# Optimization experiments

Hardware: AMD Instinct MI355X
Metric: run time of the kernel (lower is better)

## Reference

```python
import jax, jax.numpy as jnp
import numpy as np

B, S, HID = 2, 2048, 2048
N_HEADS, N_KV = 16, 8
HEAD_DIM = HID // N_HEADS  # 128
N_REP = N_HEADS // N_KV


def setup_inputs() -> dict:
    key = jax.random.key(0)
    ks = jax.random.split(key, 5)
    x = jax.random.normal(ks[0], (B, S, HID), dtype=jnp.float32)
    Wq = jax.random.normal(ks[1], (HID, N_HEADS * HEAD_DIM), dtype=jnp.float32) * 0.02
    Wk = jax.random.normal(ks[2], (HID, N_KV * HEAD_DIM), dtype=jnp.float32) * 0.02
    Wv = jax.random.normal(ks[3], (HID, N_KV * HEAD_DIM), dtype=jnp.float32) * 0.02
    Wo = jax.random.normal(ks[4], (N_HEADS * HEAD_DIM, HID), dtype=jnp.float32) * 0.02
    # standard RoPE frequencies: theta_i = 10000^(-2i/head_dim), angle = pos * theta_i
    inv_freq = 1.0 / (10000.0 ** (jnp.arange(0, HEAD_DIM, 2, dtype=jnp.float32) / HEAD_DIM))
    angles = jnp.arange(S, dtype=jnp.float32)[:, None] * inv_freq[None, :]  # [S, HEAD_DIM/2]
    return {
        "x": x, "Wq": Wq, "Wk": Wk, "Wv": Wv, "Wo": Wo,
        "freqs_cos": jnp.cos(angles), "freqs_sin": jnp.sin(angles),
        "start_pos": 0,
    }


def _rope(t, cos, sin):
    # t: [B, S, h, head_dim]; complex-view pairs are (even, odd) along last dim
    tr = t.reshape(*t.shape[:-1], -1, 2)
    re, im = tr[..., 0], tr[..., 1]
    cos = cos[None, :, None, :]
    sin = sin[None, :, None, :]
    out_re = re * cos - im * sin
    out_im = re * sin + im * cos
    return jnp.stack([out_re, out_im], axis=-1).reshape(t.shape)


def reference(x, Wq, Wk, Wv, Wo, freqs_cos, freqs_sin, start_pos):
    b, s, _ = x.shape
    xq = (x @ Wq).reshape(b, s, N_HEADS, HEAD_DIM)
    xk = (x @ Wk).reshape(b, s, N_KV, HEAD_DIM)
    xv = (x @ Wv).reshape(b, s, N_KV, HEAD_DIM)
    xq = _rope(xq, freqs_cos, freqs_sin)
    xk = _rope(xk, freqs_cos, freqs_sin)
    # repeat_kv: each kv head duplicated n_rep times consecutively
    xk = jnp.repeat(xk, N_REP, axis=2)  # [b, s, N_HEADS, hd]
    xv = jnp.repeat(xv, N_REP, axis=2)
    scale = 1.0 / jnp.sqrt(jnp.float32(HEAD_DIM))
    attn = jnp.einsum("bqhd,bkhd->bhqk", xq, xk) * scale
    attn = jax.nn.softmax(attn, axis=-1)
    out = jnp.einsum("bhqk,bkhd->bqhd", attn, xv).reshape(b, s, N_HEADS * HEAD_DIM)
    return out @ Wo
```

## Files before the change

### kernel.cpp

```cpp
#include <hip/hip_runtime.h>
#include <stdint.h>

#define DI __device__ __forceinline__

typedef unsigned short u16;
typedef unsigned int   u32;
typedef __attribute__((ext_vector_type(8))) short short8;
typedef __attribute__((ext_vector_type(4))) float f32x4;


DI u16 f2bf(float f) {
    u32 u = __float_as_uint(f);
    u32 r = u + 0x7fff + ((u >> 16) & 1);
    return (u16)(r >> 16);
}
DI u32 pk2bf(float a, float b) {
    return (u32)f2bf(a) | ((u32)f2bf(b) << 16);
}
DI float bf2f(u16 h) { return __uint_as_float(((u32)h) << 16); }

DI f32x4 mfma16(short8 a, short8 b, f32x4 c) {
    return __builtin_amdgcn_mfma_f32_16x16x32_bf16(a, b, c, 0, 0, 0);
}

DI void gload_lds16(const void* g, void* l) {
    __builtin_amdgcn_global_load_lds(
        (const __attribute__((address_space(1))) void*)g,
        (__attribute__((address_space(3))) void*)l, 16, 0, 0);
}

DI short8 rope8(short8 raw, const float* cp, const float* sp, float osc) {
    float4 c4 = *(const float4*)cp;
    float4 s4 = *(const float4*)sp;
    u32* rp = (u32*)&raw;
#pragma unroll
    for (int p = 0; p < 4; p++) {
        u32 v = rp[p];
        float re = __uint_as_float(v << 16);
        float im = __uint_as_float(v & 0xffff0000u);
        float cc = ((const float*)&c4)[p] * osc;
        float ss = ((const float*)&s4)[p] * osc;
        rp[p] = pk2bf(re * cc - im * ss, re * ss + im * cc);
    }
    return raw;
}

__global__ __launch_bounds__(256) void cvt_x(const float* __restrict__ x,
                                             u16* __restrict__ o, int n4) {
    int i = blockIdx.x * 256 + threadIdx.x;
    if (i >= n4) return;
    float4 v = *(const float4*)(x + (size_t)i * 4);
    uint2 p; p.x = pk2bf(v.x, v.y); p.y = pk2bf(v.z, v.w);
    *(uint2*)(o + (size_t)i * 4) = p;
}

__global__ __launch_bounds__(256) void transpose_cvt4(const float* __restrict__ W0,
                                                      const float* __restrict__ W1,
                                                      const float* __restrict__ W2,
                                                      const float* __restrict__ W3,
                                                      u16* __restrict__ D0,
                                                      u16* __restrict__ D1,
                                                      u16* __restrict__ D2,
                                                      u16* __restrict__ D3) {
    const float* W; u16* D; int N;
    switch (blockIdx.z) {
        case 0:  W = W0; D = D0; N = 2048; break;
        case 1:  W = W1; D = D1; N = 1024; break;
        case 2:  W = W2; D = D2; N = 1024; break;
        default: W = W3; D = D3; N = 2048; break;
    }
    if ((int)blockIdx.x >= (N >> 6)) return;
    const int K = 2048;
    __shared__ u16 tl[64][65];
    int tx = threadIdx.x & 15, ty = threadIdx.x >> 4;
    int tc = blockIdx.x * 64, tr = blockIdx.y * 64;
#pragma unroll
    for (int i = 0; i < 4; i++) {
        int r = tr + ty + i * 16;
        float4 v = *(const float4*)&W[(size_t)r * N + tc + tx * 4];
        tl[tx*4+0][ty+i*16] = f2bf(v.x);
        tl[tx*4+1][ty+i*16] = f2bf(v.y);
        tl[tx*4+2][ty+i*16] = f2bf(v.z);
        tl[tx*4+3][ty+i*16] = f2bf(v.w);
    }
    __syncthreads();
#pragma unroll
    for (int i = 0; i < 4; i++) {
        int n = tc + ty + i * 16;
        uint2 p;
        p.x = (u32)tl[ty+i*16][tx*4+0] | ((u32)tl[ty+i*16][tx*4+1] << 16);
        p.y = (u32)tl[ty+i*16][tx*4+2] | ((u32)tl[ty+i*16][tx*4+3] << 16);
        *(uint2*)&D[(size_t)n * K + tr + tx * 4] = p;
    }
}

__global__ __launch_bounds__(256) void rope_kernel(u16* __restrict__ buf,
                                                   const float* __restrict__ fc,
                                                   const float* __restrict__ fs,
                                                   int H, int tokshift, int total,
                                                   float oscale) {
    int idx = blockIdx.x * 256 + threadIdx.x;
    if (idx >= total) return;
    int tok = idx >> tokshift;
    int rem = idx & ((1 << tokshift) - 1);
    int h = rem >> 6, j = rem & 63;
    int s = tok & 2047;
    size_t a = ((size_t)tok * H + h) * 128 + 2 * j;
    u32 v = *(u32*)(buf + a);
    float re = bf2f((u16)(v & 0xffff));
    float im = bf2f((u16)(v >> 16));
    float c = fc[s * 64 + j], sn = fs[s * 64 + j];
    *(u32*)(buf + a) = pk2bf((re * c - im * sn) * oscale,
                             (re * sn + im * c) * oscale);
}

__global__ __launch_bounds__(512) void gemm_qkv8(const u16* __restrict__ A,
                                                 const u16* __restrict__ BT,
                                                 u16* __restrict__ Qo,
                                                 u16* __restrict__ Ko,
                                                 u16* __restrict__ Vo) {
    __shared__ __align__(16) u16 SM[65536];
    char* smb = (char*)SM;
    const int tid = threadIdx.x;
    const int w = tid >> 6, l = tid & 63;
    const int l15 = l & 15, lh = l >> 4;
    const int wr = w >> 2, wc = w & 3;

    const int bid = blockIdx.x;
    const int sw = (bid & 7) * 32 + (bid >> 3);
    const int bx = sw & 15, by = sw >> 4;

    const char* Ag = (const char*)A  + (size_t)(by * 256) * 4096;
    const char* Bg = (const char*)BT + (size_t)(bx * 256) * 4096;

    const int r0 = tid >> 3;
    const int c0 = ((tid & 7) << 4) ^ (((tid >> 5) & 1) << 5);
    const int wb = w << 10;

#define STG_A(tt, bb, hh) do {                                              \
        const char* s_ = Ag + (size_t)((hh) * 128 + r0) * 4096 + (tt) * 128 + c0; \
        char* d_ = smb + (bb) * 65536 + (hh) * 16384 + wb;                  \
        gload_lds16(s_, d_);                                                \
        gload_lds16(s_ + (size_t)64 * 4096, d_ + 8192);                     \
    } while (0)
#define STG_B(tt, bb, hh) do {                                              \
        const char* s_ = Bg + (size_t)((hh) * 128 + r0) * 4096 + (tt) * 128 + c0; \
        char* d_ = smb + (bb) * 65536 + 32768 + (hh) * 16384 + wb;          \
        gload_lds16(s_, d_);                                                \
        gload_lds16(s_ + (size_t)64 * 4096, d_ + 8192);                     \
    } while (0)

    const int aoff = l15 * 128 + ((lh * 16) ^ (((l15 >> 2) & 1) << 5));

    const f32x4 fz = {0.f, 0.f, 0.f, 0.f};
    f32x4 acc[8][4];
#pragma unroll
    for (int m = 0; m < 8; m++)
#pragma unroll
        for (int n = 0; n < 4; n++) acc[m][n] = fz;

    STG_A(0, 0, 0); STG_A(0, 0, 1); STG_B(0, 0, 0); STG_B(0, 0, 1);
    STG_A(1, 1, 0);
    asm volatile("s_waitcnt vmcnt(2)" ::: "memory");
    __builtin_amdgcn_s_barrier();

    for (int t = 0; t < 32; ++t) {
        const int cur = t & 1;
        const int t1 = t + 1 < 32 ? t + 1 : 31;
        const int t2 = t + 2 < 32 ? t + 2 : 31;
        const char* Ab = smb + cur * 65536 + wr * 16384 + aoff;
        const char* Bb = smb + cur * 65536 + 32768 + (wc >> 1) * 16384
                         + (wc & 1) * 8192 + aoff;
        short8 aF[4][2], bF[4][2];

        STG_A(t1, cur ^ 1, 1);
#pragma unroll
        for (int m = 0; m < 4; m++) {
            aF[m][0] = *(const short8*)(Ab + m * 2048);
            aF[m][1] = *(const short8*)(Ab + m * 2048 + 64);
        }
#pragma unroll
        for (int n = 0; n < 2; n++) {
            bF[n][0] = *(const short8*)(Bb + n * 2048);
            bF[n][1] = *(const short8*)(Bb + n * 2048 + 64);
        }
        __builtin_amdgcn_s_setprio(1);
#pragma unroll
        for (int m = 0; m < 4; m++)
#pragma unroll
            for (int n = 0; n < 2; n++) {
                acc[m][n] = mfma16(aF[m][0], bF[n][0], acc[m][n]);
                acc[m][n] = mfma16(aF[m][1], bF[n][1], acc[m][n]);
            }
        __builtin_amdgcn_s_setprio(0);
        __builtin_amdgcn_s_barrier();

        STG_B(t1, cur ^ 1, 0);
#pragma unroll
        for (int n = 2; n < 4; n++) {
            bF[n][0] = *(const short8*)(Bb + n * 2048);
            bF[n][1] = *(const short8*)(Bb + n * 2048 + 64);
        }
        __builtin_amdgcn_s_setprio(1);
#pragma unroll
        for (int m = 0; m < 4; m++)
#pragma unroll
            for (int n = 2; n < 4; n++) {
                acc[m][n] = mfma16(aF[m][0], bF[n][0], acc[m][n]);
                acc[m][n] = mfma16(aF[m][1], bF[n][1], acc[m][n]);
            }
        __builtin_amdgcn_s_setprio(0);
        __builtin_amdgcn_s_barrier();

        STG_B(t1, cur ^ 1, 1);
#pragma unroll
        for (int m = 0; m < 4; m++) {
            aF[m][0] = *(const short8*)(Ab + (m + 4) * 2048);
            aF[m][1] = *(const short8*)(Ab + (m + 4) * 2048 + 64);
        }
        __builtin_amdgcn_s_setprio(1);
#pragma unroll
        for (int m = 0; m < 4; m++)
#pragma unroll
            for (int n = 0; n < 2; n++) {
                acc[m + 4][n] = mfma16(aF[m][0], bF[n][0], acc[m + 4][n]);
                acc[m + 4][n] = mfma16(aF[m][1], bF[n][1], acc[m + 4][n]);
            }
        __builtin_amdgcn_s_setprio(0);
        __builtin_amdgcn_s_barrier();

        STG_A(t2, cur, 0);
        __builtin_amdgcn_s_setprio(1);
#pragma unroll
        for (int m = 0; m < 4; m++)
#pragma unroll
            for (int n = 2; n < 4; n++) {
                acc[m + 4][n] = mfma16(aF[m][0], bF[n][0], acc[m + 4][n]);
                acc[m + 4][n] = mfma16(aF[m][1], bF[n][1], acc[m + 4][n]);
            }
        __builtin_amdgcn_s_setprio(0);
        asm volatile("s_waitcnt vmcnt(2)" ::: "memory");
        __builtin_amdgcn_s_barrier();
    }
#undef STG_A
#undef STG_B

    const int rbase = by * 256 + wr * 128 + lh * 4;
    const int cbase = bx * 256 + wc * 64 + l15;
    if (bx < 8) {
#pragma unroll
        for (int m = 0; m < 8; m++)
#pragma unroll
            for (int j = 0; j < 4; j++) {
                size_t ro = (size_t)(rbase + m * 16 + j) * 2048 + cbase;
#pragma unroll
                for (int n = 0; n < 4; n++)
                    Qo[ro + n * 16] = f2bf(acc[m][n][j]);
            }
    } else if (bx < 12) {
        const int ck = cbase - 2048;
#pragma unroll
        for (int m = 0; m < 8; m++)
#pragma unroll
            for (int j = 0; j < 4; j++) {
                size_t ro = (size_t)(rbase + m * 16 + j) * 1024 + ck;
#pragma unroll
                for (int n = 0; n < 4; n++)
                    Ko[ro + n * 16] = f2bf(acc[m][n][j]);
            }
    } else {
#pragma unroll
        for (int m = 0; m < 8; m++)
#pragma unroll
            for (int n = 0; n < 4; n++) {
                int tok = rbase + m * 16;
                int c = cbase + n * 16 - 3072;
                int bb2 = tok >> 11, ss = tok & 2047;
                int h2 = c >> 7, d = c & 127;
                uint2 v;
                v.x = pk2bf(acc[m][n][0], acc[m][n][1]);
                v.y = pk2bf(acc[m][n][2], acc[m][n][3]);
                *(uint2*)(Vo + (size_t)((bb2 * 8 + h2) * 128 + d) * 2048 + ss) = v;
            }
    }
}

__global__ __launch_bounds__(512) void gemm_wo8(const u16* __restrict__ A,
                                                const u16* __restrict__ BT,
                                                float* __restrict__ Of) {
    __shared__ __align__(16) u16 SM[49152];
    char* smb = (char*)SM;
    const int tid = threadIdx.x;
    const int w = tid >> 6, l = tid & 63;
    const int l15 = l & 15, lh = l >> 4;
    const int wr = w >> 2, wc = w & 3;

    const int bid = blockIdx.x;
    const int sw = (bid & 7) * 32 + (bid >> 3);
    const int bx = sw & 7, by = sw >> 3;

    const char* Ag = (const char*)A  + (size_t)(by * 128) * 4096;
    const char* Bg = (const char*)BT + (size_t)(bx * 256) * 4096;

    const int r0 = tid >> 3;
    const int c0 = ((tid & 7) << 4) ^ (((tid >> 5) & 1) << 5);
    const int wb = w << 10;

#define STG_WA(tt, bb) do {                                                 \
        const char* s_ = Ag + (size_t)r0 * 4096 + (tt) * 128 + c0;          \
        char* d_ = smb + (bb) * 49152 + wb;                                 \
        gload_lds16(s_, d_);                                                \
        gload_lds16(s_ + (size_t)64 * 4096, d_ + 8192);                     \
    } while (0)
#define STG_WB(tt, bb) do {                                                 \
        const char* s_ = Bg + (size_t)r0 * 4096 + (tt) * 128 + c0;          \
        char* d_ = smb + (bb) * 49152 + 16384 + wb;                         \
        gload_lds16(s_, d_);                                                \
        gload_lds16(s_ + (size_t)64 * 4096, d_ + 8192);                     \
        gload_lds16(s_ + (size_t)128 * 4096, d_ + 16384);                   \
        gload_lds16(s_ + (size_t)192 * 4096, d_ + 24576);                   \
    } while (0)

    const int aoff = l15 * 128 + ((lh * 16) ^ (((l15 >> 2) & 1) << 5));

    const f32x4 fz = {0.f, 0.f, 0.f, 0.f};
    f32x4 acc[4][4];
#pragma unroll
    for (int m = 0; m < 4; m++)
#pragma unroll
        for (int n = 0; n < 4; n++) acc[m][n] = fz;

    STG_WA(0, 0); STG_WB(0, 0);
    STG_WA(1, 1);
    asm volatile("s_waitcnt vmcnt(2)" ::: "memory");
    __builtin_amdgcn_s_barrier();

    for (int t = 0; t < 32; ++t) {
        const int cur = t & 1;
        const int t1 = t + 1 < 32 ? t + 1 : 31;
        const int t2 = t + 2 < 32 ? t + 2 : 31;
        const char* Ab = smb + cur * 49152 + wr * 8192 + aoff;
        const char* Bb = smb + cur * 49152 + 16384 + wc * 8192 + aoff;
        short8 aF[4][2], bF[4][2];

        STG_WB(t1, cur ^ 1);
#pragma unroll
        for (int m = 0; m < 4; m++) {
            aF[m][0] = *(const short8*)(Ab + m * 2048);
            aF[m][1] = *(const short8*)(Ab + m * 2048 + 64);
        }
#pragma unroll
        for (int n = 0; n < 2; n++) {
            bF[n][0] = *(const short8*)(Bb + n * 2048);
            bF[n][1] = *(const short8*)(Bb + n * 2048 + 64);
        }
        __builtin_amdgcn_s_setprio(1);
#pragma unroll
        for (int m = 0; m < 4; m++)
#pragma unroll
            for (int n = 0; n < 2; n++) {
                acc[m][n] = mfma16(aF[m][0], bF[n][0], acc[m][n]);
                acc[m][n] = mfma16(aF[m][1], bF[n][1], acc[m][n]);
            }
        __builtin_amdgcn_s_setprio(0);
        __builtin_amdgcn_s_barrier();

        STG_WA(t2, cur);
#pragma unroll
        for (int n = 2; n < 4; n++) {
            bF[n][0] = *(const short8*)(Bb + n * 2048);
            bF[n][1] = *(const short8*)(Bb + n * 2048 + 64);
        }
        __builtin_amdgcn_s_setprio(1);
#pragma unroll
        for (int m = 0; m < 4; m++)
#pragma unroll
            for (int n = 2; n < 4; n++) {
                acc[m][n] = mfma16(aF[m][0], bF[n][0], acc[m][n]);
                acc[m][n] = mfma16(aF[m][1], bF[n][1], acc[m][n]);
            }
        __builtin_amdgcn_s_setprio(0);
        asm volatile("s_waitcnt vmcnt(2)" ::: "memory");
        __builtin_amdgcn_s_barrier();
    }
#undef STG_WA
#undef STG_WB

    const int rbase = by * 128 + wr * 64 + lh * 4;
    const int cbase = bx * 256 + wc * 64 + l15;
#pragma unroll
    for (int m = 0; m < 4; m++)
#pragma unroll
        for (int j = 0; j < 4; j++) {
            size_t ro = (size_t)(rbase + m * 16 + j) * 2048 + cbase;
#pragma unroll
            for (int n = 0; n < 4; n++)
                Of[ro + n * 16] = acc[m][n][j];
        }
}

__global__ __launch_bounds__(256, 2) void attn_kernel(const u16* __restrict__ Q,
                                                      const u16* __restrict__ Kg,
                                                      const u16* __restrict__ Vg,
                                                      const float* __restrict__ fc,
                                                      const float* __restrict__ fs,
                                                      u16* __restrict__ O) {
    __shared__ __align__(16) u16 Ks[2][8192];
    __shared__ __align__(16) u16 Vs[2][8192];
    __shared__ __align__(16) u16 Ps[4][2048];
    const int tid = threadIdx.x;
    const int w = tid >> 6, l = tid & 63;
    const int qt = blockIdx.x, bh = blockIdx.y;
    const int b = bh >> 4, h = bh & 15, h2 = h >> 1;
    const int l15 = l & 15, lh = l >> 4;

    char* KsB = (char*)&Ks[0][0];
    char* VsB = (char*)&Vs[0][0];
    char* PsB = (char*)&Ps[w][0];

    const char* Kbase = (const char*)Kg + (size_t)b * 2048 * 2048 + h2 * 256;
    const char* Vbase = (const char*)Vg + (size_t)(b * 8 + h2) * 128 * 4096;
    int krow[4], kcol[4], vrow[4], vcol[4];
#pragma unroll
    for (int c = 0; c < 4; c++) {
        int X = c * 4096 + tid * 16;
        krow[c] = X >> 8; kcol[c] = (X & 255) ^ ((krow[c] & 7) << 4);
        vrow[c] = X >> 7; vcol[c] = (X & 127) ^ ((vrow[c] & 7) << 4);
    }

#define STAGE(t, pb) do {                                               \
        const char* Kt = Kbase + (size_t)(t) * 131072;                  \
        const char* Vt = Vbase + (t) * 128;                             \
        char* kd = KsB + (pb) * 16384 + tid * 16;                       \
        char* vd = VsB + (pb) * 16384 + tid * 16;                       \
        _Pragma("unroll")                                               \
        for (int c = 0; c < 4; c++) {                                   \
            gload_lds16(Kt + krow[c] * 2048 + kcol[c], kd + c * 4096);  \
            gload_lds16(Vt + (size_t)vrow[c] * 4096 + vcol[c], vd + c * 4096); \
        }                                                               \
    } while (0)

    const float OSC = 0.12751742987f;
    short8 qf0[4], qf1[4];
    {
        const int s0r = qt * 128 + w * 32 + l15;
        const int s1r = s0r + 16;
        const u16* qp0 = Q + ((size_t)(b * 2048 + s0r)) * 2048 + h * 128 + lh * 8;
        const u16* qp1 = Q + ((size_t)(b * 2048 + s1r)) * 2048 + h * 128 + lh * 8;
#pragma unroll
        for (int ks = 0; ks < 4; ks++) {
            qf0[ks] = rope8(*(const short8*)(qp0 + ks * 32),
                            &fc[s0r * 64 + ks * 16 + lh * 4],
                            &fs[s0r * 64 + ks * 16 + lh * 4], OSC);
            qf1[ks] = rope8(*(const short8*)(qp1 + ks * 32),
                            &fc[s1r * 64 + ks * 16 + lh * 4],
                            &fs[s1r * 64 + ks * 16 + lh * 4], OSC);
        }
    }

    const f32x4 fz = {0.f, 0.f, 0.f, 0.f};
    f32x4 o0[8], o1[8];
#pragma unroll
    for (int n = 0; n < 8; n++) { o0[n] = fz; o1[n] = fz; }
    float mrow0[4] = {-1e30f, -1e30f, -1e30f, -1e30f};
    float mrow1[4] = {-1e30f, -1e30f, -1e30f, -1e30f};
    float lsum0[4] = {0.f, 0.f, 0.f, 0.f};
    float lsum1[4] = {0.f, 0.f, 0.f, 0.f};

    STAGE(0, 0);

    for (int t = 0; t < 32; t++) {
        __syncthreads();
        const int pb = t & 1;
        if (t < 31) STAGE(t + 1, pb ^ 1);
        const char* kc = KsB + pb * 16384;
        const char* vc = VsB + pb * 16384;
        const int swz = (l15 & 7) << 4;

        f32x4 s0[4], s1[4];
#pragma unroll
        for (int ct = 0; ct < 4; ct++) {
            s0[ct] = fz; s1[ct] = fz;
#pragma unroll
            for (int ks = 0; ks < 4; ks++) {
                short8 kf = *(const short8*)(kc + ((ct * 16 + l15) << 8)
                                                + ((ks * 64 + lh * 16) ^ swz));
                s0[ct] = mfma16(qf0[ks], kf, s0[ct]);
                s1[ct] = mfma16(qf1[ks], kf, s1[ct]);
            }
        }

        float pl0[4], pl1[4];
#pragma unroll
        for (int r = 0; r < 4; r++) {
            pl0[r] = fmaxf(fmaxf(s0[0][r], s0[1][r]), fmaxf(s0[2][r], s0[3][r]));
            pl1[r] = fmaxf(fmaxf(s1[0][r], s1[1][r]), fmaxf(s1[2][r], s1[3][r]));
        }
        bool grow = false;
#pragma unroll
        for (int r = 0; r < 4; r++)
            grow = grow || (pl0[r] > mrow0[r] + 8.f) || (pl1[r] > mrow1[r] + 8.f);
        if (__any(grow)) {
#pragma unroll
            for (int r = 0; r < 4; r++) {
                float mx = pl0[r];
                mx = fmaxf(mx, __shfl_xor(mx, 1));
                mx = fmaxf(mx, __shfl_xor(mx, 2));
                mx = fmaxf(mx, __shfl_xor(mx, 4));
                mx = fmaxf(mx, __shfl_xor(mx, 8));
                float mnew = fmaxf(mrow0[r], mx);
                float fsc = exp2f(mrow0[r] - mnew);
                mrow0[r] = mnew;
                lsum0[r] *= fsc;
#pragma unroll
                for (int n = 0; n < 8; n++) o0[n][r] *= fsc;
            }
#pragma unroll
            for (int r = 0; r < 4; r++) {
                float mx = pl1[r];
                mx = fmaxf(mx, __shfl_xor(mx, 1));
                mx = fmaxf(mx, __shfl_xor(mx, 2));
                mx = fmaxf(mx, __shfl_xor(mx, 4));
                mx = fmaxf(mx, __shfl_xor(mx, 8));
                float mnew = fmaxf(mrow1[r], mx);
                float fsc = exp2f(mrow1[r] - mnew);
                mrow1[r] = mnew;
                lsum1[r] *= fsc;
#pragma unroll
                for (int n = 0; n < 8; n++) o1[n][r] *= fsc;
            }
        }
        const int cb2 = l15 << 1;
#pragma unroll
        for (int r = 0; r < 4; r++) {
            float p0 = exp2f(s0[0][r] - mrow0[r]);
            float p1 = exp2f(s0[1][r] - mrow0[r]);
            float p2 = exp2f(s0[2][r] - mrow0[r]);
            float p3 = exp2f(s0[3][r] - mrow0[r]);
            lsum0[r] += (p0 + p1) + (p2 + p3);
            const int rw = lh * 4 + r;
            const int rb = rw << 7;
            const int sw2 = (rw & 7) << 4;
            *(u16*)(PsB + (rb + (( 0 + cb2) ^ sw2))) =
                (u16)((__float_as_uint(p0) + 0x8000u) >> 16);
            *(u16*)(PsB + (rb + ((32 + cb2) ^ sw2))) =
                (u16)((__float_as_uint(p1) + 0x8000u) >> 16);
            *(u16*)(PsB + (rb + ((64 + cb2) ^ sw2))) =
                (u16)((__float_as_uint(p2) + 0x8000u) >> 16);
            *(u16*)(PsB + (rb + ((96 + cb2) ^ sw2))) =
                (u16)((__float_as_uint(p3) + 0x8000u) >> 16);
        }
#pragma unroll
        for (int r = 0; r < 4; r++) {
            float p0 = exp2f(s1[0][r] - mrow1[r]);
            float p1 = exp2f(s1[1][r] - mrow1[r]);
            float p2 = exp2f(s1[2][r] - mrow1[r]);
            float p3 = exp2f(s1[3][r] - mrow1[r]);
            lsum1[r] += (p0 + p1) + (p2 + p3);
            const int rw = 16 + lh * 4 + r;
            const int rb = rw << 7;
            const int sw2 = (rw & 7) << 4;
            *(u16*)(PsB + (rb + (( 0 + cb2) ^ sw2))) =
                (u16)((__float_as_uint(p0) + 0x8000u) >> 16);
            *(u16*)(PsB + (rb + ((32 + cb2) ^ sw2))) =
                (u16)((__float_as_uint(p1) + 0x8000u) >> 16);
            *(u16*)(PsB + (rb + ((64 + cb2) ^ sw2))) =
                (u16)((__float_as_uint(p2) + 0x8000u) >> 16);
            *(u16*)(PsB + (rb + ((96 + cb2) ^ sw2))) =
                (u16)((__float_as_uint(p3) + 0x8000u) >> 16);
        }

#pragma unroll
        for (int ks2 = 0; ks2 < 2; ks2++) {
            short8 pf0 = *(const short8*)(PsB + ((l15 << 7)
                                + ((ks2 * 64 + lh * 16) ^ swz)));
            short8 pf1 = *(const short8*)(PsB + (((16 + l15) << 7)
                                + ((ks2 * 64 + lh * 16) ^ swz)));
#pragma unroll
            for (int n = 0; n < 8; n++) {
                short8 vf = *(const short8*)(vc + (((n * 16 + l15) << 7)
                                                  + ((ks2 * 64 + lh * 16) ^ swz)));
                o0[n] = mfma16(pf0, vf, o0[n]);
                o1[n] = mfma16(pf1, vf, o1[n]);
            }
        }
    }

    const int q0 = qt * 128 + w * 32;
    const size_t ob0 = ((size_t)(b * 2048 + q0 + lh * 4)) * 2048 + h * 128 + l15;
#pragma unroll
    for (int r = 0; r < 4; r++) {
        float ls = lsum0[r];
        ls += __shfl_xor(ls, 1);
        ls += __shfl_xor(ls, 2);
        ls += __shfl_xor(ls, 4);
        ls += __shfl_xor(ls, 8);
        float li = 1.0f / ls;
#pragma unroll
        for (int n = 0; n < 8; n++)
            O[ob0 + (size_t)r * 2048 + n * 16] = f2bf(o0[n][r] * li);
    }
    const size_t ob1 = ob0 + (size_t)16 * 2048;
#pragma unroll
    for (int r = 0; r < 4; r++) {
        float ls = lsum1[r];
        ls += __shfl_xor(ls, 1);
        ls += __shfl_xor(ls, 2);
        ls += __shfl_xor(ls, 4);
        ls += __shfl_xor(ls, 8);
        float li = 1.0f / ls;
#pragma unroll
        for (int n = 0; n < 8; n++)
            O[ob1 + (size_t)r * 2048 + n * 16] = f2bf(o1[n][r] * li);
    }
#undef STAGE
}

extern "C" void kernel_launch(void* const* d_in, const int* in_sizes, int n_in,
                              void* d_out, int out_size, void* d_ws, size_t ws_size,
                              hipStream_t stream) {
    const float* x  = (const float*)d_in[0];
    const float* Wq = (const float*)d_in[1];
    const float* Wk = (const float*)d_in[2];
    const float* Wv = (const float*)d_in[3];
    const float* Wo = (const float*)d_in[4];
    const float* fc = (const float*)d_in[5];
    const float* fs = (const float*)d_in[6];
    float* out = (float*)d_out;

    uint8_t* ws = (uint8_t*)d_ws;
    u16* xb   = (u16*)(ws + 0);
    u16* wqkv = (u16*)(ws + 16777216);
    u16* wqT  = (u16*)(ws + 16777216);
    u16* wkT  = (u16*)(ws + 25165824);
    u16* wvT  = (u16*)(ws + 29360128);
    u16* woT  = (u16*)(ws + 33554432);
    u16* qb   = (u16*)(ws + 41943040);
    u16* kb   = (u16*)(ws + 58720256);
    u16* vT   = (u16*)(ws + 67108864);
    u16* ao   = xb;

    cvt_x<<<dim3(8192), dim3(256), 0, stream>>>(x, xb, 2097152);
    transpose_cvt4<<<dim3(32, 32, 4), dim3(256), 0, stream>>>(Wq, Wk, Wv, Wo,
                                                              wqT, wkT, wvT, woT);

    gemm_qkv8<<<dim3(256), dim3(512), 0, stream>>>(xb, wqkv, qb, kb, vT);

    rope_kernel<<<dim3(8192), dim3(256), 0, stream>>>(kb, fc, fs, 8, 9, 2097152, 1.0f);

    attn_kernel<<<dim3(16, 32), dim3(256), 0, stream>>>(qb, kb, vT, fc, fs, ao);

    gemm_wo8<<<dim3(256), dim3(512), 0, stream>>>(ao, woT, out);
}
```

Baseline: 233.3 us.

## Shrink QKV GEMM tile to 128x256 and launch 512 blocks

The fused QKV projection GEMM tile drops from 256x256 to 128x256 rows per block, doubling the grid to 512 workgroups. Each block now stages one A half-tile and the full B tile per k-step, with two compute phases instead of four, and uses less LDS. The goal is to fill all 256 CUs more evenly and cut the wave-quantization tail. The cost is lower arithmetic intensity per block, so B-operand global and LDS traffic rises for each FLOP.

```diff
diff --git a/kernel.cpp b/kernel.cpp
--- a/kernel.cpp
+++ b/kernel.cpp
@@ -114,12 +114,12 @@
                              (re * sn + im * c) * oscale);
 }
 
-__global__ __launch_bounds__(512) void gemm_qkv8(const u16* __restrict__ A,
+__global__ __launch_bounds__(512) void gemm_qkv2(const u16* __restrict__ A,
                                                  const u16* __restrict__ BT,
                                                  u16* __restrict__ Qo,
                                                  u16* __restrict__ Ko,
                                                  u16* __restrict__ Vo) {
-    __shared__ __align__(16) u16 SM[65536];
+    __shared__ __align__(16) u16 SM[49152];
     char* smb = (char*)SM;
     const int tid = threadIdx.x;
     const int w = tid >> 6, l = tid & 63;
@@ -127,40 +127,42 @@
     const int wr = w >> 2, wc = w & 3;
 
     const int bid = blockIdx.x;
-    const int sw = (bid & 7) * 32 + (bid >> 3);
+    const int sw = (bid & 7) * 64 + (bid >> 3);
     const int bx = sw & 15, by = sw >> 4;
 
-    const char* Ag = (const char*)A  + (size_t)(by * 256) * 4096;
+    const char* Ag = (const char*)A  + (size_t)(by * 128) * 4096;
     const char* Bg = (const char*)BT + (size_t)(bx * 256) * 4096;
 
     const int r0 = tid >> 3;
     const int c0 = ((tid & 7) << 4) ^ (((tid >> 5) & 1) << 5);
     const int wb = w << 10;
 
-#define STG_A(tt, bb, hh) do {                                              \
-        const char* s_ = Ag + (size_t)((hh) * 128 + r0) * 4096 + (tt) * 128 + c0; \
-        char* d_ = smb + (bb) * 65536 + (hh) * 16384 + wb;                  \
+#define STG_WA(tt, bb) do {                                                 \
+        const char* s_ = Ag + (size_t)r0 * 4096 + (tt) * 128 + c0;          \
+        char* d_ = smb + (bb) * 49152 + wb;                                 \
         gload_lds16(s_, d_);                                                \
         gload_lds16(s_ + (size_t)64 * 4096, d_ + 8192);                     \
     } while (0)
-#define STG_B(tt, bb, hh) do {                                              \
-        const char* s_ = Bg + (size_t)((hh) * 128 + r0) * 4096 + (tt) * 128 + c0; \
-        char* d_ = smb + (bb) * 65536 + 32768 + (hh) * 16384 + wb;          \
+#define STG_WB(tt, bb) do {                                                 \
+        const char* s_ = Bg + (size_t)r0 * 4096 + (tt) * 128 + c0;          \
+        char* d_ = smb + (bb) * 49152 + 16384 + wb;                         \
         gload_lds16(s_, d_);                                                \
         gload_lds16(s_ + (size_t)64 * 4096, d_ + 8192);                     \
+        gload_lds16(s_ + (size_t)128 * 4096, d_ + 16384);                   \
+        gload_lds16(s_ + (size_t)192 * 4096, d_ + 24576);                   \
     } while (0)
 
     const int aoff = l15 * 128 + ((lh * 16) ^ (((l15 >> 2) & 1) << 5));
 
     const f32x4 fz = {0.f, 0.f, 0.f, 0.f};
-    f32x4 acc[8][4];
-#pragma unroll
-    for (int m = 0; m < 8; m++)
+    f32x4 acc[4][4];
+#pragma unroll
+    for (int m = 0; m < 4; m++)
 #pragma unroll
         for (int n = 0; n < 4; n++) acc[m][n] = fz;
 
-    STG_A(0, 0, 0); STG_A(0, 0, 1); STG_B(0, 0, 0); STG_B(0, 0, 1);
-    STG_A(1, 1, 0);
+    STG_WA(0, 0); STG_WB(0, 0);
+    STG_WA(1, 1);
     asm volatile("s_waitcnt vmcnt(2)" ::: "memory");
     __builtin_amdgcn_s_barrier();
 
@@ -168,12 +170,11 @@
         const int cur = t & 1;
         const int t1 = t + 1 < 32 ? t + 1 : 31;
         const int t2 = t + 2 < 32 ? t + 2 : 31;
-        const char* Ab = smb + cur * 65536 + wr * 16384 + aoff;
-        const char* Bb = smb + cur * 65536 + 32768 + (wc >> 1) * 16384
-                         + (wc & 1) * 8192 + aoff;
+        const char* Ab = smb + cur * 49152 + wr * 8192 + aoff;
+        const char* Bb = smb + cur * 49152 + 16384 + wc * 8192 + aoff;
         short8 aF[4][2], bF[4][2];
 
-        STG_A(t1, cur ^ 1, 1);
+        STG_WB(t1, cur ^ 1);
 #pragma unroll
         for (int m = 0; m < 4; m++) {
             aF[m][0] = *(const short8*)(Ab + m * 2048);
@@ -195,7 +196,7 @@
         __builtin_amdgcn_s_setprio(0);
         __builtin_amdgcn_s_barrier();
 
-        STG_B(t1, cur ^ 1, 0);
+        STG_WA(t2, cur);
 #pragma unroll
         for (int n = 2; n < 4; n++) {
             bF[n][0] = *(const short8*)(Bb + n * 2048);
@@ -210,46 +211,17 @@
                 acc[m][n] = mfma16(aF[m][1], bF[n][1], acc[m][n]);
             }
         __builtin_amdgcn_s_setprio(0);
-        __builtin_amdgcn_s_barrier();
-
-        STG_B(t1, cur ^ 1, 1);
-#pragma unroll
-        for (int m = 0; m < 4; m++) {
-            aF[m][0] = *(const short8*)(Ab + (m + 4) * 2048);
-            aF[m][1] = *(const short8*)(Ab + (m + 4) * 2048 + 64);
-        }
-        __builtin_amdgcn_s_setprio(1);
-#pragma unroll
-        for (int m = 0; m < 4; m++)
-#pragma unroll
-            for (int n = 0; n < 2; n++) {
-                acc[m + 4][n] = mfma16(aF[m][0], bF[n][0], acc[m + 4][n]);
-                acc[m + 4][n] = mfma16(aF[m][1], bF[n][1], acc[m + 4][n]);
-            }
-        __builtin_amdgcn_s_setprio(0);
-        __builtin_amdgcn_s_barrier();
-
-        STG_A(t2, cur, 0);
-        __builtin_amdgcn_s_setprio(1);
-#pragma unroll
-        for (int m = 0; m < 4; m++)
-#pragma unroll
-            for (int n = 2; n < 4; n++) {
-                acc[m + 4][n] = mfma16(aF[m][0], bF[n][0], acc[m + 4][n]);
-                acc[m + 4][n] = mfma16(aF[m][1], bF[n][1], acc[m + 4][n]);
-            }
-        __builtin_amdgcn_s_setprio(0);
         asm volatile("s_waitcnt vmcnt(2)" ::: "memory");
         __builtin_amdgcn_s_barrier();
     }
-#undef STG_A
-#undef STG_B
-
-    const int rbase = by * 256 + wr * 128 + lh * 4;
+#undef STG_WA
+#undef STG_WB
+
+    const int rbase = by * 128 + wr * 64 + lh * 4;
     const int cbase = bx * 256 + wc * 64 + l15;
     if (bx < 8) {
 #pragma unroll
-        for (int m = 0; m < 8; m++)
+        for (int m = 0; m < 4; m++)
 #pragma unroll
             for (int j = 0; j < 4; j++) {
                 size_t ro = (size_t)(rbase + m * 16 + j) * 2048 + cbase;
@@ -260,7 +232,7 @@
     } else if (bx < 12) {
         const int ck = cbase - 2048;
 #pragma unroll
-        for (int m = 0; m < 8; m++)
+        for (int m = 0; m < 4; m++)
 #pragma unroll
             for (int j = 0; j < 4; j++) {
                 size_t ro = (size_t)(rbase + m * 16 + j) * 1024 + ck;
@@ -270,7 +242,7 @@
             }
     } else {
 #pragma unroll
-        for (int m = 0; m < 8; m++)
+        for (int m = 0; m < 4; m++)
 #pragma unroll
             for (int n = 0; n < 4; n++) {
                 int tok = rbase + m * 16;
@@ -644,7 +616,7 @@
     transpose_cvt4<<<dim3(32, 32, 4), dim3(256), 0, stream>>>(Wq, Wk, Wv, Wo,
                                                               wqT, wkT, wvT, woT);
 
-    gemm_qkv8<<<dim3(256), dim3(512), 0, stream>>>(xb, wqkv, qb, kb, vT);
+    gemm_qkv2<<<dim3(512), dim3(512), 0, stream>>>(xb, wqkv, qb, kb, vT);
 
     rope_kernel<<<dim3(8192), dim3(256), 0, stream>>>(kb, fc, fs, 8, 9, 2097152, 1.0f);
 
```

Result: slower. 246.6 us (+5.7%).
